# Kernel optimization log

Measured on AMD Instinct MI355X. Metric: run time of the kernel, lower is better.

The kernel has to match this reference:

```python
import jax, jax.numpy as jnp
import numpy as np

COLS = 8
D = 128
B = 8192
NUM_EMB = 12
PAIRS = [(i, j) for i in range(COLS) for j in range(COLS) if i < j]  # 28 column pairs


def setup_inputs() -> dict:
    key = jax.random.key(0)
    ks = jax.random.split(key, 7)
    return {
        "features": jax.random.randint(ks[0], (COLS, B), 0, NUM_EMB),
        "emb_mean": jax.random.normal(ks[1], (COLS, NUM_EMB, D), jnp.float32),
        "emb_std": jax.random.normal(ks[2], (COLS, NUM_EMB, D), jnp.float32),
        "W_nc": jax.random.normal(ks[3], (len(PAIRS), 4, 2, D), jnp.float32) * 0.05,
        "W_cat": jax.random.normal(ks[4], (len(PAIRS), 2, 2 * D), jnp.float32) * 0.05,
        "log_alpha": jax.random.normal(ks[5], (len(PAIRS), 5), jnp.float32),
        "noise": jax.random.normal(ks[6], (len(PAIRS), 2, B, D), jnp.float32),
    }


def reference(features, emb_mean, emb_std, W_nc, W_cat, log_alpha, noise):
    # Gather all column embeddings once: [COLS, B, D]
    col_idx = jnp.arange(COLS)[:, None]
    M = emb_mean[col_idx, features]
    S = jax.nn.softplus(emb_std[col_idx, features])  # torch.log(1+exp(std))
    pos = jnp.argmax(log_alpha, axis=-1)  # [28] hard top-1 routing per pair
    inferences = jnp.zeros((features.shape[1], 2), M.dtype)
    for k, (i, j) in enumerate(PAIRS):
        # reparameterize: mu + softplus(std) * noise * 0.01 (fresh noise per call)
        p = M[i] + S[i] * noise[k, 0] * 0.01
        q = M[j] + S[j] * noise[k, 1] * 0.01
        branches = [
            lambda p, q, k=k: (p + q) @ W_nc[k, 0].T,
            lambda p, q, k=k: (p * q) @ W_nc[k, 1].T,
            lambda p, q, k=k: jnp.maximum(p, q) @ W_nc[k, 2].T,
            lambda p, q, k=k: jnp.minimum(p, q) @ W_nc[k, 3].T,
            lambda p, q, k=k: jnp.concatenate([p, q], axis=-1) @ W_cat[k].T,
        ]
        # weights is one-hot (scatter of argmax) so weights[pos] == 1.0
        inferences = inferences + jax.lax.switch(pos[k], branches, p, q)
    return inferences  # [B, 2]
```

## Files before the change

kernel.cpp:

```cpp
#include <hip/hip_runtime.h>

constexpr int COLS    = 8;
constexpr int BATCH   = 8192;
constexpr int D       = 128;
constexpr int NUM_EMB = 12;
constexpr int NPAIRS  = 28;

constexpr int CHUNKS        = 32;
constexpr int ROWS_PER_CHUNK = BATCH / CHUNKS;
constexpr size_t HSTRIDE = (size_t)BATCH * D;

typedef float floatx4 __attribute__((ext_vector_type(4)));

__device__ const int PI_d[NPAIRS] = {0,0,0,0,0,0,0, 1,1,1,1,1,1, 2,2,2,2,2, 3,3,3,3, 4,4,4, 5,5, 6};
__device__ const int PJ_d[NPAIRS] = {1,2,3,4,5,6,7, 2,3,4,5,6,7, 3,4,5,6,7, 4,5,6,7, 5,6,7, 6,7, 7};

__device__ __forceinline__ floatx4 ld4(const float* p) {
    return *reinterpret_cast<const floatx4*>(p);
}
__device__ __forceinline__ void st4(float* p, floatx4 v) {
    *reinterpret_cast<floatx4*>(p) = v;
}
__device__ __forceinline__ float dot4(floatx4 a, floatx4 b) {
    return fmaf(a.x, b.x, fmaf(a.y, b.y, fmaf(a.z, b.z, a.w * b.w)));
}
__device__ __forceinline__ floatx4 vmax4(floatx4 a, floatx4 b) {
    floatx4 r; r.x=fmaxf(a.x,b.x); r.y=fmaxf(a.y,b.y); r.z=fmaxf(a.z,b.z); r.w=fmaxf(a.w,b.w); return r;
}
__device__ __forceinline__ floatx4 vmin4(floatx4 a, floatx4 b) {
    floatx4 r; r.x=fminf(a.x,b.x); r.y=fminf(a.y,b.y); r.z=fminf(a.z,b.z); r.w=fminf(a.w,b.w); return r;
}

__global__ __launch_bounds__(256) void sp_kernel(const float* __restrict__ emb_std,
                                                 float* __restrict__ spstd)
{
    const int idx = blockIdx.x * 256 + threadIdx.x;
    if (idx < COLS * NUM_EMB * D / 4) {
        const floatx4 v = ld4(emb_std + 4 * idx);
        floatx4 r;
        r.x = 0.01f * ((v.x > 15.0f) ? v.x : log1pf(expf(v.x)));
        r.y = 0.01f * ((v.y > 15.0f) ? v.y : log1pf(expf(v.y)));
        r.z = 0.01f * ((v.z > 15.0f) ? v.z : log1pf(expf(v.z)));
        r.w = 0.01f * ((v.w > 15.0f) ? v.w : log1pf(expf(v.w)));
        st4(spstd + 4 * idx, r);
    }
}

template<int S, bool ATOMIC>
__device__ __forceinline__ void row_loop(
    int k, int chunk, int halfid, int lane, int d0,
    const int* __restrict__ fI, const int* __restrict__ fJ,
    const float* __restrict__ miB, const float* __restrict__ siB,
    const float* __restrict__ mjB, const float* __restrict__ sjB,
    const float* __restrict__ nk0, const float* __restrict__ nk1,
    floatx4 A0, floatx4 B0, floatx4 A1, floatx4 B1,
    float* __restrict__ dst)
{
    #pragma unroll 2
    for (int r = 0; r < ROWS_PER_CHUNK / 8; ++r) {
        const int b = chunk * ROWS_PER_CHUNK + r * 8 + halfid;

        const floatx4 n0 = ld4(nk0 + (size_t)b * D);
        const floatx4 n1 = ld4(nk1 + (size_t)b * D);

        const int fi = fI[b];
        const int fj = fJ[b];
        const floatx4 Mi = ld4(miB + fi * D);
        const floatx4 Si = ld4(siB + fi * D);
        const floatx4 Mj = ld4(mjB + fj * D);
        const floatx4 Sj = ld4(sjB + fj * D);

        const floatx4 p = Mi + Si * n0;
        const floatx4 q = Mj + Sj * n1;

        float a0, a1;
        if constexpr (S == 4) {
            a0 = dot4(p, A0) + dot4(q, B0);
            a1 = dot4(p, A1) + dot4(q, B1);
        } else {
            floatx4 c;
            if constexpr (S == 0)      c = p + q;
            else if constexpr (S == 1) c = p * q;
            else if constexpr (S == 2) c = vmax4(p, q);
            else                       c = vmin4(p, q);
            a0 = dot4(c, A0);
            a1 = dot4(c, A1);
        }

        #pragma unroll
        for (int m = 16; m >= 1; m >>= 1) {
            a0 += __shfl_xor(a0, m, 64);
            a1 += __shfl_xor(a1, m, 64);
        }

        if (lane == 0) {
            if constexpr (ATOMIC) {
                atomicAdd(dst + b * 2 + 0, a0);
                atomicAdd(dst + b * 2 + 1, a1);
            } else {
                float2 r2; r2.x = a0; r2.y = a1;
                *reinterpret_cast<float2*>(dst + ((size_t)k * BATCH + b) * 2) = r2;
            }
        }
    }
}

template<bool ATOMIC>
__global__ __launch_bounds__(256) void pair_kernel(
    const int*   __restrict__ features,
    const float* __restrict__ emb_mean,
    const float* __restrict__ spstd,
    const float* __restrict__ W_nc,
    const float* __restrict__ W_cat,
    const float* __restrict__ log_alpha,
    const float* __restrict__ noise,
    float*       __restrict__ dst)
{
    const int bid    = blockIdx.x;
    const int k      = bid >> 5;
    const int chunk  = bid & (CHUNKS - 1);
    const int tid    = threadIdx.x;
    const int halfid = tid >> 5;
    const int lane   = tid & 31;
    const int d0     = lane * 4;

    const float* la = log_alpha + k * 5;
    float best = la[0];
    int   s    = 0;
    #pragma unroll
    for (int t = 1; t < 5; ++t) {
        const float v = la[t];
        if (v > best) { best = v; s = t; }
    }

    floatx4 A0 = {0,0,0,0}, B0 = {0,0,0,0}, A1 = {0,0,0,0}, B1 = {0,0,0,0};
    if (s == 4) {
        const float* wb = W_cat + (size_t)k * 512;
        A0 = ld4(wb + d0);       B0 = ld4(wb + 128 + d0);
        A1 = ld4(wb + 256 + d0); B1 = ld4(wb + 384 + d0);
    } else {
        const float* wb = W_nc + (size_t)(k * 4 + s) * 256;
        A0 = ld4(wb + d0);
        A1 = ld4(wb + 128 + d0);
    }

    const int i = PI_d[k];
    const int j = PJ_d[k];
    const int* fI = features + i * BATCH;
    const int* fJ = features + j * BATCH;
    const float* miB = emb_mean + (size_t)i * NUM_EMB * D + d0;
    const float* siB = spstd    + (size_t)i * NUM_EMB * D + d0;
    const float* mjB = emb_mean + (size_t)j * NUM_EMB * D + d0;
    const float* sjB = spstd    + (size_t)j * NUM_EMB * D + d0;
    const float* nk0 = noise + (size_t)(2 * k) * HSTRIDE + d0;
    const float* nk1 = nk0 + HSTRIDE;

    switch (s) {
        case 0: row_loop<0,ATOMIC>(k,chunk,halfid,lane,d0,fI,fJ,miB,siB,mjB,sjB,nk0,nk1,A0,B0,A1,B1,dst); break;
        case 1: row_loop<1,ATOMIC>(k,chunk,halfid,lane,d0,fI,fJ,miB,siB,mjB,sjB,nk0,nk1,A0,B0,A1,B1,dst); break;
        case 2: row_loop<2,ATOMIC>(k,chunk,halfid,lane,d0,fI,fJ,miB,siB,mjB,sjB,nk0,nk1,A0,B0,A1,B1,dst); break;
        case 3: row_loop<3,ATOMIC>(k,chunk,halfid,lane,d0,fI,fJ,miB,siB,mjB,sjB,nk0,nk1,A0,B0,A1,B1,dst); break;
        default:row_loop<4,ATOMIC>(k,chunk,halfid,lane,d0,fI,fJ,miB,siB,mjB,sjB,nk0,nk1,A0,B0,A1,B1,dst); break;
    }
}

__global__ __launch_bounds__(256) void reduce_kernel(const float* __restrict__ partial,
                                                     float* __restrict__ out)
{
    const int idx = blockIdx.x * 256 + threadIdx.x;
    float s = 0.0f;
    #pragma unroll
    for (int k = 0; k < NPAIRS; ++k) {
        s += partial[(size_t)k * (BATCH * 2) + idx];
    }
    out[idx] = s;
}

__global__ __launch_bounds__(256) void zero_kernel(float* __restrict__ out)
{
    const int idx = blockIdx.x * 256 + threadIdx.x;
    out[idx] = 0.0f;
}

extern "C" void kernel_launch(void* const* d_in, const int* in_sizes, int n_in,
                              void* d_out, int out_size, void* d_ws, size_t ws_size,
                              hipStream_t stream) {
    const int*   features  = (const int*)  d_in[0];
    const float* emb_mean  = (const float*)d_in[1];
    const float* emb_std   = (const float*)d_in[2];
    const float* W_nc      = (const float*)d_in[3];
    const float* W_cat     = (const float*)d_in[4];
    const float* log_alpha = (const float*)d_in[5];
    const float* noise     = (const float*)d_in[6];
    float*       out       = (float*)d_out;

    float* spstd   = (float*)d_ws;
    float* partial = spstd + COLS * NUM_EMB * D;
    const size_t need_bytes = (size_t)(COLS * NUM_EMB * D + NPAIRS * BATCH * 2) * 4;

    sp_kernel<<<dim3(12), dim3(256), 0, stream>>>(emb_std, spstd);

    if (ws_size >= need_bytes) {
        pair_kernel<false><<<dim3(NPAIRS * CHUNKS), dim3(256), 0, stream>>>(
            features, emb_mean, spstd, W_nc, W_cat, log_alpha, noise, partial);
        reduce_kernel<<<dim3(BATCH * 2 / 256), dim3(256), 0, stream>>>(partial, out);
    } else {
        zero_kernel<<<dim3(BATCH * 2 / 256), dim3(256), 0, stream>>>(out);
        pair_kernel<true><<<dim3(NPAIRS * CHUNKS), dim3(256), 0, stream>>>(
            features, emb_mean, spstd, W_nc, W_cat, log_alpha, noise, out);
    }
}
```

Before: 49.73 us.

## Fuse softplus into pair kernel via shared memory and double chunk count

Drops the separate softplus kernel launch. Each block now computes softplus of its two columns' std tables into shared memory, and the gather loop reads Si/Sj from LDS instead of global. Chunks per pair go from 32 to 64 (1792 blocks) and the row-loop unroll rises from 2 to 4. This removes one launch and its dependency, at the cost of redundant softplus work per block plus a __syncthreads before the loop.

```diff
diff --git a/kernel.cpp b/kernel.cpp
--- a/kernel.cpp
+++ b/kernel.cpp
@@ -6,7 +6,7 @@
 constexpr int NUM_EMB = 12;
 constexpr int NPAIRS  = 28;
 
-constexpr int CHUNKS        = 32;
+constexpr int CHUNKS         = 64;
 constexpr int ROWS_PER_CHUNK = BATCH / CHUNKS;
 constexpr size_t HSTRIDE = (size_t)BATCH * D;
 
@@ -30,33 +30,21 @@
 __device__ __forceinline__ floatx4 vmin4(floatx4 a, floatx4 b) {
     floatx4 r; r.x=fminf(a.x,b.x); r.y=fminf(a.y,b.y); r.z=fminf(a.z,b.z); r.w=fminf(a.w,b.w); return r;
 }
-
-__global__ __launch_bounds__(256) void sp_kernel(const float* __restrict__ emb_std,
-                                                 float* __restrict__ spstd)
-{
-    const int idx = blockIdx.x * 256 + threadIdx.x;
-    if (idx < COLS * NUM_EMB * D / 4) {
-        const floatx4 v = ld4(emb_std + 4 * idx);
-        floatx4 r;
-        r.x = 0.01f * ((v.x > 15.0f) ? v.x : log1pf(expf(v.x)));
-        r.y = 0.01f * ((v.y > 15.0f) ? v.y : log1pf(expf(v.y)));
-        r.z = 0.01f * ((v.z > 15.0f) ? v.z : log1pf(expf(v.z)));
-        r.w = 0.01f * ((v.w > 15.0f) ? v.w : log1pf(expf(v.w)));
-        st4(spstd + 4 * idx, r);
-    }
+__device__ __forceinline__ float softplus01(float x) {
+    return 0.01f * ((x > 15.0f) ? x : log1pf(expf(x)));
 }
 
 template<int S, bool ATOMIC>
 __device__ __forceinline__ void row_loop(
     int k, int chunk, int halfid, int lane, int d0,
     const int* __restrict__ fI, const int* __restrict__ fJ,
-    const float* __restrict__ miB, const float* __restrict__ siB,
-    const float* __restrict__ mjB, const float* __restrict__ sjB,
+    const float* __restrict__ miB, const float* __restrict__ mjB,
+    const float* spI, const float* spJ,
     const float* __restrict__ nk0, const float* __restrict__ nk1,
     floatx4 A0, floatx4 B0, floatx4 A1, floatx4 B1,
     float* __restrict__ dst)
 {
-    #pragma unroll 2
+    #pragma unroll 4
     for (int r = 0; r < ROWS_PER_CHUNK / 8; ++r) {
         const int b = chunk * ROWS_PER_CHUNK + r * 8 + halfid;
 
@@ -66,9 +54,9 @@
         const int fi = fI[b];
         const int fj = fJ[b];
         const floatx4 Mi = ld4(miB + fi * D);
-        const floatx4 Si = ld4(siB + fi * D);
         const floatx4 Mj = ld4(mjB + fj * D);
-        const floatx4 Sj = ld4(sjB + fj * D);
+        const floatx4 Si = ld4(spI + fi * D);
+        const floatx4 Sj = ld4(spJ + fj * D);
 
         const floatx4 p = Mi + Si * n0;
         const floatx4 q = Mj + Sj * n1;
@@ -109,20 +97,42 @@
 __global__ __launch_bounds__(256) void pair_kernel(
     const int*   __restrict__ features,
     const float* __restrict__ emb_mean,
-    const float* __restrict__ spstd,
+    const float* __restrict__ emb_std,
     const float* __restrict__ W_nc,
     const float* __restrict__ W_cat,
     const float* __restrict__ log_alpha,
     const float* __restrict__ noise,
     float*       __restrict__ dst)
 {
+    __shared__ float spS[2][NUM_EMB][D];
+
     const int bid    = blockIdx.x;
-    const int k      = bid >> 5;
-    const int chunk  = bid & (CHUNKS - 1);
+    const int k      = bid / CHUNKS;
+    const int chunk  = bid % CHUNKS;
     const int tid    = threadIdx.x;
     const int halfid = tid >> 5;
     const int lane   = tid & 31;
     const int d0     = lane * 4;
+
+    const int i = PI_d[k];
+    const int j = PJ_d[k];
+
+    #pragma unroll
+    for (int r = 0; r < 3; ++r) {
+        const int idx  = tid + r * 256;
+        const int col  = idx >= 384 ? 1 : 0;
+        const int rem  = idx - col * 384;
+        const int e    = rem >> 5;
+        const int dd   = (rem & 31) * 4;
+        const int cidx = col ? j : i;
+        const floatx4 v = ld4(emb_std + ((size_t)(cidx * NUM_EMB + e)) * D + dd);
+        floatx4 o;
+        o.x = softplus01(v.x);
+        o.y = softplus01(v.y);
+        o.z = softplus01(v.z);
+        o.w = softplus01(v.w);
+        st4(&spS[col][e][dd], o);
+    }
 
     const float* la = log_alpha + k * 5;
     float best = la[0];
@@ -144,23 +154,23 @@
         A1 = ld4(wb + 128 + d0);
     }
 
-    const int i = PI_d[k];
-    const int j = PJ_d[k];
+    __syncthreads();
+
     const int* fI = features + i * BATCH;
     const int* fJ = features + j * BATCH;
     const float* miB = emb_mean + (size_t)i * NUM_EMB * D + d0;
-    const float* siB = spstd    + (size_t)i * NUM_EMB * D + d0;
     const float* mjB = emb_mean + (size_t)j * NUM_EMB * D + d0;
-    const float* sjB = spstd    + (size_t)j * NUM_EMB * D + d0;
+    const float* spI = &spS[0][0][0] + d0;
+    const float* spJ = &spS[1][0][0] + d0;
     const float* nk0 = noise + (size_t)(2 * k) * HSTRIDE + d0;
     const float* nk1 = nk0 + HSTRIDE;
 
     switch (s) {
-        case 0: row_loop<0,ATOMIC>(k,chunk,halfid,lane,d0,fI,fJ,miB,siB,mjB,sjB,nk0,nk1,A0,B0,A1,B1,dst); break;
-        case 1: row_loop<1,ATOMIC>(k,chunk,halfid,lane,d0,fI,fJ,miB,siB,mjB,sjB,nk0,nk1,A0,B0,A1,B1,dst); break;
-        case 2: row_loop<2,ATOMIC>(k,chunk,halfid,lane,d0,fI,fJ,miB,siB,mjB,sjB,nk0,nk1,A0,B0,A1,B1,dst); break;
-        case 3: row_loop<3,ATOMIC>(k,chunk,halfid,lane,d0,fI,fJ,miB,siB,mjB,sjB,nk0,nk1,A0,B0,A1,B1,dst); break;
-        default:row_loop<4,ATOMIC>(k,chunk,halfid,lane,d0,fI,fJ,miB,siB,mjB,sjB,nk0,nk1,A0,B0,A1,B1,dst); break;
+        case 0: row_loop<0,ATOMIC>(k,chunk,halfid,lane,d0,fI,fJ,miB,mjB,spI,spJ,nk0,nk1,A0,B0,A1,B1,dst); break;
+        case 1: row_loop<1,ATOMIC>(k,chunk,halfid,lane,d0,fI,fJ,miB,mjB,spI,spJ,nk0,nk1,A0,B0,A1,B1,dst); break;
+        case 2: row_loop<2,ATOMIC>(k,chunk,halfid,lane,d0,fI,fJ,miB,mjB,spI,spJ,nk0,nk1,A0,B0,A1,B1,dst); break;
+        case 3: row_loop<3,ATOMIC>(k,chunk,halfid,lane,d0,fI,fJ,miB,mjB,spI,spJ,nk0,nk1,A0,B0,A1,B1,dst); break;
+        default:row_loop<4,ATOMIC>(k,chunk,halfid,lane,d0,fI,fJ,miB,mjB,spI,spJ,nk0,nk1,A0,B0,A1,B1,dst); break;
     }
 }
 
@@ -194,19 +204,16 @@
     const float* noise     = (const float*)d_in[6];
     float*       out       = (float*)d_out;
 
-    float* spstd   = (float*)d_ws;
-    float* partial = spstd + COLS * NUM_EMB * D;
-    const size_t need_bytes = (size_t)(COLS * NUM_EMB * D + NPAIRS * BATCH * 2) * 4;
-
-    sp_kernel<<<dim3(12), dim3(256), 0, stream>>>(emb_std, spstd);
+    float* partial = (float*)d_ws;
+    const size_t need_bytes = (size_t)NPAIRS * BATCH * 2 * 4;
 
     if (ws_size >= need_bytes) {
         pair_kernel<false><<<dim3(NPAIRS * CHUNKS), dim3(256), 0, stream>>>(
-            features, emb_mean, spstd, W_nc, W_cat, log_alpha, noise, partial);
+            features, emb_mean, emb_std, W_nc, W_cat, log_alpha, noise, partial);
         reduce_kernel<<<dim3(BATCH * 2 / 256), dim3(256), 0, stream>>>(partial, out);
     } else {
         zero_kernel<<<dim3(BATCH * 2 / 256), dim3(256), 0, stream>>>(out);
         pair_kernel<true><<<dim3(NPAIRS * CHUNKS), dim3(256), 0, stream>>>(
-            features, emb_mean, spstd, W_nc, W_cat, log_alpha, noise, out);
-    }
-}
+            features, emb_mean, emb_std, W_nc, W_cat, log_alpha, noise, out);
+    }
+}
```

After: 50.04 us. No clear change (+0.6%).
